# Kernel tuning notes

Measured on AMD Instinct MI355X. Metric: run time of the kernel, lower is better.

The kernel has to match this reference:

```python
import jax, jax.numpy as jnp
import numpy as np
import math


def setup_inputs() -> dict:
    key = jax.random.key(0)
    k1, k2, k3, k4 = jax.random.split(key, 4)
    b, h, T, dk = 1, 8, 4096, 64
    BS = 64
    T_q = 2048
    num_blocks = T // BS
    q = jax.random.normal(k1, (b, h, T_q, dk), dtype=jnp.float32)
    k = jax.random.normal(k2, (b, h, T, dk), dtype=jnp.float32)
    v = jax.random.normal(k3, (b, h, T, dk), dtype=jnp.float32)
    top2_idx = jax.random.randint(k4, (b, h, T_q, 2), 0, num_blocks, dtype=jnp.int32)
    return {"q": q, "k": k, "v": v, "BS": BS, "top2_idx": top2_idx}


def reference(q, k, v, BS, top2_idx):
    b, h, T, dk = k.shape
    num_blocks = T // BS
    T_q = top2_idx.shape[2]
    # [b,h,num_blocks,BS,dk]
    k_blocks = k.reshape(b, h, num_blocks, BS, dk)
    v_blocks = v.reshape(b, h, num_blocks, BS, dk)
    # gather 2 blocks per query: flat idx [b,h,T_q*2] -> select along block axis
    flat_idx = top2_idx.reshape(b, h, T_q * 2)[..., None, None]  # [b,h,2*T_q,1,1]
    k_sel = jnp.take_along_axis(k_blocks, flat_idx, axis=2).reshape(b, h, T_q, 2 * BS, dk)
    v_sel = jnp.take_along_axis(v_blocks, flat_idx, axis=2).reshape(b, h, T_q, 2 * BS, dk)
    # per-query attention over its 2*BS gathered keys
    score = jnp.einsum("bhqd,bhqkd->bhqk", q, k_sel) / math.sqrt(dk)
    score = jax.nn.softmax(score, axis=-1)
    out = jnp.einsum("bhqk,bhqkd->bhqd", score, v_sel)
    return out
```

## Files before the change

### kernel.cpp

```cpp
#include <hip/hip_runtime.h>


#define NH      8
#define TQ      2048
#define TKV     4096
#define DK      64
#define BSZ     64
#define NB      (TKV / BSZ)
#define NQ_TOT  (NH * TQ)
#define NENT    (NQ_TOT * 2)
#define NBUCKET (NH * NB)
#define SSPLIT  2
#define CAP     256

#define WS_NEEDED    ((size_t)NENT * 68 * 4)

typedef __attribute__((ext_vector_type(8))) short bf16x8;
typedef __attribute__((ext_vector_type(4))) float f32x4;

__device__ __forceinline__ short f2bf(float x) {
    union { float f; unsigned u; } c; c.f = x;
    unsigned r = c.u + 0x7fffu + ((c.u >> 16) & 1u);
    return (short)(r >> 16);
}

__device__ __forceinline__ bf16x8 pack_bf16x8(float4 a, float4 b) {
    bf16x8 r;
    r[0] = f2bf(a.x); r[1] = f2bf(a.y); r[2] = f2bf(a.z); r[3] = f2bf(a.w);
    r[4] = f2bf(b.x); r[5] = f2bf(b.y); r[6] = f2bf(b.z); r[7] = f2bf(b.w);
    return r;
}

#define KSTR 72
#define VSTR 78

__global__ __launch_bounds__(256, 2) void bucket_kernel(
    const float* __restrict__ q,
    const float* __restrict__ k,
    const float* __restrict__ v,
    const int*   __restrict__ top2,
    float*       __restrict__ partials)
{
    __shared__ __align__(16) short K_lds[BSZ * KSTR];
    __shared__ __align__(16) short V_lds[BSZ * VSTR];
    __shared__ __align__(16) short P_lds[4][16 * 72];
    __shared__ int lds_list[CAP];
    __shared__ int wave_tot[4];

    const int bucket  = blockIdx.x & (NBUCKET - 1);
    const int subtile = blockIdx.x >> 9;
    const int wave = threadIdx.x >> 6;
    const int lane = threadIdx.x & 63;
    const int W    = subtile * 4 + wave;

    const int h    = bucket >> 6;
    const int blk  = bucket & (NB - 1);

    const int* th = top2 + h * (TQ * 2);
    int cnt = 0;
#pragma unroll
    for (int rep = 0; rep < (TQ * 2) / 256; ++rep) {
        if ((th[rep * 256 + threadIdx.x] & (NB - 1)) == blk) ++cnt;
    }
    int pre = cnt;
#pragma unroll
    for (int off = 1; off < 64; off <<= 1) {
        const int nb = __shfl_up(pre, off);
        if (lane >= off) pre += nb;
    }
    if (lane == 63) wave_tot[wave] = pre;
    __syncthreads();
    int wbase = 0;
#pragma unroll
    for (int wv = 0; wv < 4; ++wv) if (wv < wave) wbase += wave_tot[wv];
    int nq = wave_tot[0] + wave_tot[1] + wave_tot[2] + wave_tot[3];
    nq = (nq > CAP) ? CAP : nq;
    {
        int p = wbase + pre - cnt;
#pragma unroll
        for (int rep = 0; rep < (TQ * 2) / 256; ++rep) {
            const int i = rep * 256 + threadIdx.x;
            if ((th[i] & (NB - 1)) == blk) {
                if (p < CAP) lds_list[p] = h * (TQ * 2) + i;
                ++p;
            }
        }
    }
    __syncthreads();

    const int ntiles = (nq + 15) >> 4;
    if (ntiles <= subtile * 4) return;

    const int n16  = lane & 15;
    const int quad = lane >> 4;

    const float* kb = k + ((size_t)h * TKV + (size_t)blk * BSZ) * DK;
    const float* vb = v + ((size_t)h * TKV + (size_t)blk * BSZ) * DK;

    {
        const int row = threadIdx.x >> 2;
        const int seg = threadIdx.x & 3;
        const float* kp = kb + row * DK + seg * 16;
        const float* vp = vb + row * DK + seg * 16;
        short* kd = &K_lds[row * KSTR + seg * 16];
        short* vd = &V_lds[row * VSTR + seg * 16];
#pragma unroll
        for (int c = 0; c < 4; ++c) {
            const float4 a = *(const float4*)(kp + c * 4);
            kd[c * 4 + 0] = f2bf(a.x); kd[c * 4 + 1] = f2bf(a.y);
            kd[c * 4 + 2] = f2bf(a.z); kd[c * 4 + 3] = f2bf(a.w);
            const float4 b = *(const float4*)(vp + c * 4);
            vd[c * 4 + 0] = f2bf(b.x); vd[c * 4 + 1] = f2bf(b.y);
            vd[c * 4 + 2] = f2bf(b.z); vd[c * 4 + 3] = f2bf(b.w);
        }
    }
    __syncthreads();
    if (W >= ntiles) return;

    bf16x8 kf[4][2];
#pragma unroll
    for (int kt = 0; kt < 4; ++kt)
#pragma unroll
        for (int ks = 0; ks < 2; ++ks)
            kf[kt][ks] = *(const bf16x8*)&K_lds[(kt * 16 + n16) * KSTR + ks * 32 + quad * 8];

    bf16x8 vf[4][2];
#pragma unroll
    for (int dt = 0; dt < 4; ++dt)
#pragma unroll
        for (int ks = 0; ks < 2; ++ks) {
            bf16x8 t;
#pragma unroll
            for (int jj = 0; jj < 8; ++jj)
                t[jj] = V_lds[(ks * 32 + quad * 8 + jj) * VSTR + dt * 16 + n16];
            vf[dt][ks] = t;
        }

    short* pl = &P_lds[wave][0];

    for (int t = W; t < ntiles; t += 4 * SSPLIT) {
        const int tbase = t * 16;

        const int em_idx = (tbase + n16 < nq) ? (tbase + n16) : 0;
        const int qi = lds_list[em_idx] >> 1;
        bf16x8 qf[2];
#pragma unroll
        for (int ks = 0; ks < 2; ++ks) {
            const float* p = q + (size_t)qi * DK + ks * 32 + quad * 8;
            float4 lo = *(const float4*)p, hi = *(const float4*)(p + 4);
            lo.x *= 0.125f; lo.y *= 0.125f; lo.z *= 0.125f; lo.w *= 0.125f;
            hi.x *= 0.125f; hi.y *= 0.125f; hi.z *= 0.125f; hi.w *= 0.125f;
            qf[ks] = pack_bf16x8(lo, hi);
        }

        f32x4 acc[4];
#pragma unroll
        for (int kt = 0; kt < 4; ++kt) {
            f32x4 a = {0.f, 0.f, 0.f, 0.f};
            a = __builtin_amdgcn_mfma_f32_16x16x32_bf16(qf[0], kf[kt][0], a, 0, 0, 0);
            a = __builtin_amdgcn_mfma_f32_16x16x32_bf16(qf[1], kf[kt][1], a, 0, 0, 0);
            acc[kt] = a;
        }

        float m4[4], l4[4], P[4][4];
#pragma unroll
        for (int r = 0; r < 4; ++r) {
            float mx = fmaxf(fmaxf(acc[0][r], acc[1][r]), fmaxf(acc[2][r], acc[3][r]));
            mx = fmaxf(mx, __shfl_xor(mx, 1));
            mx = fmaxf(mx, __shfl_xor(mx, 2));
            mx = fmaxf(mx, __shfl_xor(mx, 4));
            mx = fmaxf(mx, __shfl_xor(mx, 8));
            float s = 0.f;
#pragma unroll
            for (int kt = 0; kt < 4; ++kt) { P[kt][r] = __expf(acc[kt][r] - mx); s += P[kt][r]; }
            s += __shfl_xor(s, 1);
            s += __shfl_xor(s, 2);
            s += __shfl_xor(s, 4);
            s += __shfl_xor(s, 8);
            m4[r] = mx; l4[r] = s;
        }

#pragma unroll
        for (int r = 0; r < 4; ++r)
#pragma unroll
            for (int kt = 0; kt < 4; ++kt)
                pl[(quad * 4 + r) * 72 + kt * 16 + n16] = f2bf(P[kt][r]);

        bf16x8 pf[2];
#pragma unroll
        for (int ks = 0; ks < 2; ++ks)
            pf[ks] = *(const bf16x8*)&pl[n16 * 72 + ks * 32 + quad * 8];

        f32x4 oacc[4];
#pragma unroll
        for (int dt = 0; dt < 4; ++dt) {
            f32x4 a = {0.f, 0.f, 0.f, 0.f};
            a = __builtin_amdgcn_mfma_f32_16x16x32_bf16(pf[0], vf[dt][0], a, 0, 0, 0);
            a = __builtin_amdgcn_mfma_f32_16x16x32_bf16(pf[1], vf[dt][1], a, 0, 0, 0);
            oacc[dt] = a;
        }

#pragma unroll
        for (int r = 0; r < 4; ++r) {
            const int row = tbase + quad * 4 + r;
            if (row < nq) {
                const int e = lds_list[row];
                float* pp = partials + (size_t)e * 68;
#pragma unroll
                for (int dt = 0; dt < 4; ++dt)
                    pp[dt * 16 + n16] = oacc[dt][r];
                if (n16 == 0) pp[64] = m4[r];
                if (n16 == 1) pp[65] = l4[r];
            }
        }
    }
}

__global__ __launch_bounds__(256) void combine_kernel(
    const float* __restrict__ partials, float* __restrict__ out)
{
    const int t  = blockIdx.x * 256 + threadIdx.x;
    const int qi = t >> 4;
    const int dc = t & 15;
    const float* p0 = partials + (size_t)(qi * 2) * 68;
    const float* p1 = p0 + 68;
    const float m0 = p0[64], l0 = p0[65];
    const float m1 = p1[64], l1 = p1[65];
    const float m  = fmaxf(m0, m1);
    const float a0 = __expf(m0 - m), a1 = __expf(m1 - m);
    const float inv = 1.0f / (a0 * l0 + a1 * l1);
    const float4 o0 = *(const float4*)(p0 + dc * 4);
    const float4 o1 = *(const float4*)(p1 + dc * 4);
    float4 o;
    o.x = (o0.x * a0 + o1.x * a1) * inv;
    o.y = (o0.y * a0 + o1.y * a1) * inv;
    o.z = (o0.z * a0 + o1.z * a1) * inv;
    o.w = (o0.w * a0 + o1.w * a1) * inv;
    *(float4*)(out + (size_t)qi * DK + dc * 4) = o;
}

__global__ __launch_bounds__(256) void blockattn_fallback(
    const float* __restrict__ q, const float* __restrict__ k,
    const float* __restrict__ v, const int* __restrict__ top2,
    float* __restrict__ out)
{
    const int wave = threadIdx.x >> 6;
    const int lane = threadIdx.x & 63;
    const int qidx = (blockIdx.x << 2) + wave;
    const int bh   = qidx >> 11;
    const int g    = lane >> 4;
    const int dc   = lane & 15;

    const int2 idx = *(const int2*)(top2 + (size_t)qidx * 2);
    const size_t bh_off = (size_t)bh * (TKV * DK);
    const int off = g * DK + dc * 4;

    const float* kb0 = k + bh_off + (size_t)idx.x * (BSZ * DK) + off;
    const float* kb1 = k + bh_off + (size_t)idx.y * (BSZ * DK) + off;
    const float* vb0 = v + bh_off + (size_t)idx.x * (BSZ * DK) + off;
    const float* vb1 = v + bh_off + (size_t)idx.y * (BSZ * DK) + off;
    const float4 qf = *(const float4*)(q + (size_t)qidx * DK + dc * 4);

    float sc[32];
#pragma unroll
    for (int i = 0; i < 16; ++i) {
        const float4 a = *(const float4*)(kb0 + i * 256);
        float p = a.x*qf.x + a.y*qf.y + a.z*qf.z + a.w*qf.w;
        p += __shfl_xor(p,1); p += __shfl_xor(p,2); p += __shfl_xor(p,4); p += __shfl_xor(p,8);
        sc[i] = p * 0.125f;
    }
#pragma unroll
    for (int i = 0; i < 16; ++i) {
        const float4 a = *(const float4*)(kb1 + i * 256);
        float p = a.x*qf.x + a.y*qf.y + a.z*qf.z + a.w*qf.w;
        p += __shfl_xor(p,1); p += __shfl_xor(p,2); p += __shfl_xor(p,4); p += __shfl_xor(p,8);
        sc[16+i] = p * 0.125f;
    }
    float m = sc[0];
#pragma unroll
    for (int i = 1; i < 32; ++i) m = fmaxf(m, sc[i]);
    m = fmaxf(m, __shfl_xor(m,16)); m = fmaxf(m, __shfl_xor(m,32));
    float sum = 0.f;
#pragma unroll
    for (int i = 0; i < 32; ++i) { sc[i] = __expf(sc[i]-m); sum += sc[i]; }
    sum += __shfl_xor(sum,16); sum += __shfl_xor(sum,32);
    const float inv = 1.0f / sum;

    float4 acc = make_float4(0.f,0.f,0.f,0.f);
#pragma unroll
    for (int i = 0; i < 16; ++i) {
        const float4 a = *(const float4*)(vb0 + i * 256);
        acc.x += a.x*sc[i]; acc.y += a.y*sc[i]; acc.z += a.z*sc[i]; acc.w += a.w*sc[i];
    }
#pragma unroll
    for (int i = 0; i < 16; ++i) {
        const float4 a = *(const float4*)(vb1 + i * 256);
        acc.x += a.x*sc[16+i]; acc.y += a.y*sc[16+i]; acc.z += a.z*sc[16+i]; acc.w += a.w*sc[16+i];
    }
    acc.x += __shfl_xor(acc.x,16); acc.y += __shfl_xor(acc.y,16);
    acc.z += __shfl_xor(acc.z,16); acc.w += __shfl_xor(acc.w,16);
    acc.x += __shfl_xor(acc.x,32); acc.y += __shfl_xor(acc.y,32);
    acc.z += __shfl_xor(acc.z,32); acc.w += __shfl_xor(acc.w,32);

    if (g == 0) {
        float4 o;
        o.x = acc.x*inv; o.y = acc.y*inv; o.z = acc.z*inv; o.w = acc.w*inv;
        *(float4*)(out + (size_t)qidx * DK + dc * 4) = o;
    }
}

extern "C" void kernel_launch(void* const* d_in, const int* in_sizes, int n_in,
                              void* d_out, int out_size, void* d_ws, size_t ws_size,
                              hipStream_t stream) {
    const float* q    = (const float*)d_in[0];
    const float* k    = (const float*)d_in[1];
    const float* v    = (const float*)d_in[2];
    const int*   top2 = (const int*)d_in[4];
    float*       out  = (float*)d_out;

    if (ws_size < WS_NEEDED) {
        dim3 grid(NQ_TOT / 4), block(256);
        hipLaunchKernelGGL(blockattn_fallback, grid, block, 0, stream, q, k, v, top2, out);
        return;
    }

    float* parts = (float*)d_ws;

    hipLaunchKernelGGL(bucket_kernel,  dim3(NBUCKET * SSPLIT), dim3(256), 0, stream,
                       q, k, v, top2, parts);
    hipLaunchKernelGGL(combine_kernel, dim3(NQ_TOT * 16 / 256), dim3(256), 0, stream,
                       parts, out);
}
```

Before: 83.03 us.

## Use one block per bucket, cache top2 in registers, vectorize partial stores

Removes the second subtile split, so each bucket is handled by a single block whose four waves loop over all tiles. The top2 indices are kept in registers between the count and scatter passes instead of being read twice. The 1/sqrt(dk) scale is applied to K once per bucket rather than to every Q load. The PV MFMA operands are swapped so each lane holds one query's output and can write it with float4 stores. Halving the grid roughly halves the redundant top2 scans and K/V conversions, at the cost of fewer blocks (512) and so less parallelism across the GPU.

```diff
diff --git a/kernel.cpp b/kernel.cpp
--- a/kernel.cpp
+++ b/kernel.cpp
@@ -10,7 +10,6 @@
 #define NQ_TOT  (NH * TQ)
 #define NENT    (NQ_TOT * 2)
 #define NBUCKET (NH * NB)
-#define SSPLIT  2
 #define CAP     256
 
 #define WS_NEEDED    ((size_t)NENT * 68 * 4)
@@ -47,20 +46,20 @@
     __shared__ int lds_list[CAP];
     __shared__ int wave_tot[4];
 
-    const int bucket  = blockIdx.x & (NBUCKET - 1);
-    const int subtile = blockIdx.x >> 9;
+    const int bucket = blockIdx.x;
     const int wave = threadIdx.x >> 6;
     const int lane = threadIdx.x & 63;
-    const int W    = subtile * 4 + wave;
 
     const int h    = bucket >> 6;
     const int blk  = bucket & (NB - 1);
 
     const int* th = top2 + h * (TQ * 2);
+    int tv[(TQ * 2) / 256];
     int cnt = 0;
 #pragma unroll
     for (int rep = 0; rep < (TQ * 2) / 256; ++rep) {
-        if ((th[rep * 256 + threadIdx.x] & (NB - 1)) == blk) ++cnt;
+        tv[rep] = th[rep * 256 + threadIdx.x];
+        if ((tv[rep] & (NB - 1)) == blk) ++cnt;
     }
     int pre = cnt;
 #pragma unroll
@@ -79,9 +78,8 @@
         int p = wbase + pre - cnt;
 #pragma unroll
         for (int rep = 0; rep < (TQ * 2) / 256; ++rep) {
-            const int i = rep * 256 + threadIdx.x;
-            if ((th[i] & (NB - 1)) == blk) {
-                if (p < CAP) lds_list[p] = h * (TQ * 2) + i;
+            if ((tv[rep] & (NB - 1)) == blk) {
+                if (p < CAP) lds_list[p] = h * (TQ * 2) + rep * 256 + threadIdx.x;
                 ++p;
             }
         }
@@ -89,7 +87,7 @@
     __syncthreads();
 
     const int ntiles = (nq + 15) >> 4;
-    if (ntiles <= subtile * 4) return;
+    if (ntiles == 0) return;
 
     const int n16  = lane & 15;
     const int quad = lane >> 4;
@@ -98,24 +96,27 @@
     const float* vb = v + ((size_t)h * TKV + (size_t)blk * BSZ) * DK;
 
     {
-        const int row = threadIdx.x >> 2;
-        const int seg = threadIdx.x & 3;
-        const float* kp = kb + row * DK + seg * 16;
-        const float* vp = vb + row * DK + seg * 16;
-        short* kd = &K_lds[row * KSTR + seg * 16];
-        short* vd = &V_lds[row * VSTR + seg * 16];
-#pragma unroll
-        for (int c = 0; c < 4; ++c) {
-            const float4 a = *(const float4*)(kp + c * 4);
-            kd[c * 4 + 0] = f2bf(a.x); kd[c * 4 + 1] = f2bf(a.y);
-            kd[c * 4 + 2] = f2bf(a.z); kd[c * 4 + 3] = f2bf(a.w);
-            const float4 b = *(const float4*)(vp + c * 4);
-            vd[c * 4 + 0] = f2bf(b.x); vd[c * 4 + 1] = f2bf(b.y);
-            vd[c * 4 + 2] = f2bf(b.z); vd[c * 4 + 3] = f2bf(b.w);
+#pragma unroll
+        for (int uu = 0; uu < 2; ++uu) {
+            const int u   = threadIdx.x + uu * 256;
+            const int row = u >> 3;
+            const int j   = u & 7;
+            const float* kp = kb + row * DK + j * 8;
+            float4 a = *(const float4*)kp;
+            float4 b = *(const float4*)(kp + 4);
+            a.x *= 0.125f; a.y *= 0.125f; a.z *= 0.125f; a.w *= 0.125f;
+            b.x *= 0.125f; b.y *= 0.125f; b.z *= 0.125f; b.w *= 0.125f;
+            *(bf16x8*)&K_lds[row * KSTR + j * 8] = pack_bf16x8(a, b);
+            const float* vp = vb + row * DK + j * 8;
+            const float4 c = *(const float4*)vp;
+            const float4 d = *(const float4*)(vp + 4);
+            short* vd = &V_lds[row * VSTR + j * 8];
+            vd[0] = f2bf(c.x); vd[1] = f2bf(c.y); vd[2] = f2bf(c.z); vd[3] = f2bf(c.w);
+            vd[4] = f2bf(d.x); vd[5] = f2bf(d.y); vd[6] = f2bf(d.z); vd[7] = f2bf(d.w);
         }
     }
     __syncthreads();
-    if (W >= ntiles) return;
+    if (wave >= ntiles) return;
 
     bf16x8 kf[4][2];
 #pragma unroll
@@ -138,7 +139,7 @@
 
     short* pl = &P_lds[wave][0];
 
-    for (int t = W; t < ntiles; t += 4 * SSPLIT) {
+    for (int t = wave; t < ntiles; t += 4) {
         const int tbase = t * 16;
 
         const int em_idx = (tbase + n16 < nq) ? (tbase + n16) : 0;
@@ -147,9 +148,8 @@
 #pragma unroll
         for (int ks = 0; ks < 2; ++ks) {
             const float* p = q + (size_t)qi * DK + ks * 32 + quad * 8;
-            float4 lo = *(const float4*)p, hi = *(const float4*)(p + 4);
-            lo.x *= 0.125f; lo.y *= 0.125f; lo.z *= 0.125f; lo.w *= 0.125f;
-            hi.x *= 0.125f; hi.y *= 0.125f; hi.z *= 0.125f; hi.w *= 0.125f;
+            const float4 lo = *(const float4*)p;
+            const float4 hi = *(const float4*)(p + 4);
             qf[ks] = pack_bf16x8(lo, hi);
         }
 
@@ -195,22 +195,31 @@
 #pragma unroll
         for (int dt = 0; dt < 4; ++dt) {
             f32x4 a = {0.f, 0.f, 0.f, 0.f};
-            a = __builtin_amdgcn_mfma_f32_16x16x32_bf16(pf[0], vf[dt][0], a, 0, 0, 0);
-            a = __builtin_amdgcn_mfma_f32_16x16x32_bf16(pf[1], vf[dt][1], a, 0, 0, 0);
+            a = __builtin_amdgcn_mfma_f32_16x16x32_bf16(vf[dt][0], pf[0], a, 0, 0, 0);
+            a = __builtin_amdgcn_mfma_f32_16x16x32_bf16(vf[dt][1], pf[1], a, 0, 0, 0);
             oacc[dt] = a;
         }
 
-#pragma unroll
-        for (int r = 0; r < 4; ++r) {
-            const int row = tbase + quad * 4 + r;
-            if (row < nq) {
-                const int e = lds_list[row];
+        {
+            const int rowq = tbase + n16;
+            if (rowq < nq) {
+                const int e = lds_list[rowq];
                 float* pp = partials + (size_t)e * 68;
 #pragma unroll
                 for (int dt = 0; dt < 4; ++dt)
-                    pp[dt * 16 + n16] = oacc[dt][r];
-                if (n16 == 0) pp[64] = m4[r];
-                if (n16 == 1) pp[65] = l4[r];
+                    *(f32x4*)(pp + dt * 16 + quad * 4) = oacc[dt];
+            }
+        }
+        if (n16 < 2) {
+#pragma unroll
+            for (int r = 0; r < 4; ++r) {
+                const int row4 = tbase + quad * 4 + r;
+                if (row4 < nq) {
+                    const int e = lds_list[row4];
+                    float* pp = partials + (size_t)e * 68;
+                    if (n16 == 0) pp[64] = m4[r];
+                    else          pp[65] = l4[r];
+                }
             }
         }
     }
@@ -326,7 +335,7 @@
 
     float* parts = (float*)d_ws;
 
-    hipLaunchKernelGGL(bucket_kernel,  dim3(NBUCKET * SSPLIT), dim3(256), 0, stream,
+    hipLaunchKernelGGL(bucket_kernel,  dim3(NBUCKET), dim3(256), 0, stream,
                        q, k, v, top2, parts);
     hipLaunchKernelGGL(combine_kernel, dim3(NQ_TOT * 16 / 256), dim3(256), 0, stream,
                        parts, out);
```

New measurement: 83.09 us. Within noise of the previous version (+0.1%).
